# Performance work log

Measured on AMD Instinct MI355X. Metric: run time of the kernel, lower is better.

The kernel has to match this reference:

```python
import jax, jax.numpy as jnp
import numpy as np

DIM = 1024
HEADS = 8
DIM_HEAD = 64
INNER = HEADS * DIM_HEAD
SCALE = DIM_HEAD ** -0.5


def setup_inputs() -> dict:
    key = jax.random.key(0)
    ks = jax.random.split(key, 6)
    b, n = 2, 2048
    x = jax.random.normal(ks[0], (b, n, DIM), dtype=jnp.float32)
    rel_pos_bias = jax.random.normal(ks[1], (HEADS, n, n), dtype=jnp.float32)
    # learned params (Linear stores W as [out, in]; we keep [in, out] for x @ W)
    Wq = jax.random.normal(ks[2], (DIM, INNER), dtype=jnp.float32) * (DIM ** -0.5)
    Wkv = jax.random.normal(ks[3], (DIM, 2 * DIM_HEAD), dtype=jnp.float32) * (DIM ** -0.5)
    Wo = jax.random.normal(ks[4], (INNER, DIM), dtype=jnp.float32) * (INNER ** -0.5)
    bo = jax.random.normal(ks[5], (DIM,), dtype=jnp.float32) * 0.01
    return {"x": x, "rel_pos_bias": rel_pos_bias, "Wq": Wq, "Wkv": Wkv, "Wo": Wo, "bo": bo}


def reference(x, rel_pos_bias, Wq, Wkv, Wo, bo):
    b, n, _ = x.shape
    q = x @ Wq                       # [b, n, h*d]
    kv = x @ Wkv                     # [b, n, 2d] (multi-query: single shared kv head)
    k, v = kv[..., :DIM_HEAD], kv[..., DIM_HEAD:]
    q = q.reshape(b, n, HEADS, DIM_HEAD).transpose(0, 2, 1, 3) * SCALE  # [b, h, n, d]
    sim = jnp.einsum('bhid,bjd->bhij', q, k)
    sim = sim + rel_pos_bias         # bias broadcast over batch
    causal_mask = jnp.triu(jnp.ones((n, n), dtype=bool), k=1)
    neg = -jnp.finfo(sim.dtype).max
    sim = jnp.where(causal_mask, neg, sim)
    attn = jax.nn.softmax(sim, axis=-1)  # stable softmax (max-subtract internally)
    out = jnp.einsum('bhij,bjd->bhid', attn, v)
    out = out.transpose(0, 2, 1, 3).reshape(b, n, INNER)  # [b, n, h*d]
    return out @ Wo + bo
```

## Files before the change

kernel.cpp:

```cpp
#include <hip/hip_runtime.h>

#define NSEQ 2048
#define NB 2
#define NH 8
#define HD 64
#define DMODEL 1024
#define DINNER 512

#define SLOT_F 4224
#define LOG2E 1.44269504f

typedef __attribute__((ext_vector_type(8))) short bf16x8;
typedef __attribute__((ext_vector_type(4))) float f32x4;

__device__ __forceinline__ ushort f2bf(float f) {
  uint u = __float_as_uint(f);
  uint r = (u + 0x7fffu + ((u >> 16) & 1u)) >> 16;
  return (ushort)r;
}

__device__ __forceinline__ void gld16(const ushort* g, ushort* l) {
  __builtin_amdgcn_global_load_lds(
      (const __attribute__((address_space(1))) uint*)g,
      (__attribute__((address_space(3))) uint*)l, 16, 0, 0);
}

__global__ __launch_bounds__(256) void transpose_cast_both_kernel(
    const float* __restrict__ Wq, const float* __restrict__ Wkv,
    const float* __restrict__ Wo, ushort* __restrict__ WT1,
    ushort* __restrict__ WoT) {
  __shared__ float t[64][65];
  const int id = blockIdx.x;
  const float *srcA, *srcB;
  int ldA, ldB, nsplit, Ktot, k0, n0;
  ushort* dst;
  if (id < 160) {
    k0 = (id & 15) * 64; n0 = (id >> 4) * 64;
    srcA = Wq; srcB = Wkv; ldA = 512; ldB = 128; nsplit = 512;
    Ktot = 1024; dst = WT1;
  } else {
    const int u = id - 160;
    k0 = (u & 7) * 64; n0 = (u >> 3) * 64;
    srcA = Wo; srcB = Wo; ldA = 1024; ldB = 1024; nsplit = 1024;
    Ktot = 512; dst = WoT;
  }
  const float* src; int ld, nb;
  if (n0 < nsplit) { src = srcA; ld = ldA; nb = n0; }
  else { src = srcB; ld = ldB; nb = n0 - nsplit; }
  const int r = threadIdx.x >> 4;
  const int c = (threadIdx.x & 15) * 4;
#pragma unroll
  for (int rr = r; rr < 64; rr += 16) {
    float4 v = *(const float4*)(src + (size_t)(k0 + rr) * ld + nb + c);
    t[rr][c + 0] = v.x; t[rr][c + 1] = v.y; t[rr][c + 2] = v.z; t[rr][c + 3] = v.w;
  }
  __syncthreads();
#pragma unroll
  for (int rr = r; rr < 64; rr += 16) {
    ushort4 o;
    o.x = f2bf(t[c + 0][rr]); o.y = f2bf(t[c + 1][rr]);
    o.z = f2bf(t[c + 2][rr]); o.w = f2bf(t[c + 3][rr]);
    *(ushort4*)(dst + (size_t)(n0 + rr) * Ktot + k0 + c) = o;
  }
}

__device__ __forceinline__ void stageA_bf16(const ushort* __restrict__ src, int ld,
                                            int row0, int k0, ushort* lds, int tid) {
#pragma unroll
  for (int i = 0; i < 4; ++i) {
    const int cix = i * 256 + tid;
    const int row = cix >> 3, j = cix & 7;
    uint4 v = *(const uint4*)(src + (size_t)(row0 + row) * ld + k0 + j * 8);
    *(uint4*)((char*)lds + row * 128 + ((j ^ (row & 7)) << 4)) = v;
  }
}
__device__ __forceinline__ void stageA_f32(const float* __restrict__ src, int ld,
                                           int row0, int k0, ushort* lds, int tid) {
#pragma unroll
  for (int i = 0; i < 4; ++i) {
    const int cix = i * 256 + tid;
    const int row = cix >> 3, j = cix & 7;
    const float* p = src + (size_t)(row0 + row) * ld + k0 + j * 8;
    float4 a = *(const float4*)p;
    float4 b = *(const float4*)(p + 4);
    uint u0, u1, u2, u3;
    asm("v_cvt_pk_bf16_f32 %0, %1, %2" : "=v"(u0) : "v"(a.x), "v"(a.y));
    asm("v_cvt_pk_bf16_f32 %0, %1, %2" : "=v"(u1) : "v"(a.z), "v"(a.w));
    asm("v_cvt_pk_bf16_f32 %0, %1, %2" : "=v"(u2) : "v"(b.x), "v"(b.y));
    asm("v_cvt_pk_bf16_f32 %0, %1, %2" : "=v"(u3) : "v"(b.z), "v"(b.w));
    uint4 v; v.x = u0; v.y = u1; v.z = u2; v.w = u3;
    *(uint4*)((char*)lds + row * 128 + ((j ^ (row & 7)) << 4)) = v;
  }
}
__device__ __forceinline__ void stageB(const ushort* __restrict__ src, int ld,
                                       int row0, int k0, ushort* lds, int tid) {
#pragma unroll
  for (int i = 0; i < 2; ++i) {
    const int cix = i * 256 + tid;
    const int row = cix >> 3, j = cix & 7;
    uint4 v = *(const uint4*)(src + (size_t)(row0 + row) * ld + k0 + j * 8);
    *(uint4*)((char*)lds + row * 128 + ((j ^ (row & 7)) << 4)) = v;
  }
}

__global__ __launch_bounds__(256) void qkv_mfma_kernel(
    const float* __restrict__ x, const ushort* __restrict__ WT1,
    ushort* __restrict__ qb, ushort* __restrict__ ksw, ushort* __restrict__ vsw) {
  __shared__ ushort As[128 * 64];
  __shared__ ushort Bs[64 * 64];
  const int tid = threadIdx.x;
  const int m0 = blockIdx.x * 128, n0 = blockIdx.y * 64;
  const int lane = tid & 63;
  const int w = tid >> 6;
  const int wr = w >> 1, wc = w & 1;
  const int lr = lane & 15, lg = lane >> 4;
  f32x4 acc[4][2];
#pragma unroll
  for (int a = 0; a < 4; ++a)
#pragma unroll
    for (int b = 0; b < 2; ++b) acc[a][b] = (f32x4){0.f, 0.f, 0.f, 0.f};
  for (int k0 = 0; k0 < DMODEL; k0 += 64) {
    __syncthreads();
    stageA_f32(x, DMODEL, m0, k0, As, tid);
    stageB(WT1, DMODEL, n0, k0, Bs, tid);
    __syncthreads();
#pragma unroll
    for (int kk = 0; kk < 2; ++kk) {
      bf16x8 af[4], bfr[2];
#pragma unroll
      for (int mi = 0; mi < 4; ++mi) {
        const int r = wr * 64 + mi * 16 + lr;
        af[mi] = *(const bf16x8*)((char*)As + r * 128 + (((kk * 4 + lg) ^ (r & 7)) << 4));
      }
#pragma unroll
      for (int ni = 0; ni < 2; ++ni) {
        const int r = wc * 32 + ni * 16 + lr;
        bfr[ni] = *(const bf16x8*)((char*)Bs + r * 128 + (((kk * 4 + lg) ^ (r & 7)) << 4));
      }
#pragma unroll
      for (int mi = 0; mi < 4; ++mi)
#pragma unroll
        for (int ni = 0; ni < 2; ++ni)
          acc[mi][ni] = __builtin_amdgcn_mfma_f32_16x16x32_bf16(af[mi], bfr[ni],
                                                                acc[mi][ni], 0, 0, 0);
    }
  }
#pragma unroll
  for (int mi = 0; mi < 4; ++mi)
#pragma unroll
    for (int ni = 0; ni < 2; ++ni) {
      const int n = n0 + wc * 32 + ni * 16 + lr;
#pragma unroll
      for (int r = 0; r < 4; ++r) {
        const int m = m0 + wr * 64 + mi * 16 + lg * 4 + r;
        const int bb = m >> 11, key = m & (NSEQ - 1);
        const float v = acc[mi][ni][r];
        if (blockIdx.y < 8) {
          const int h = n >> 6, d = n & 63;
          qb[((size_t)((bb * NH + h) * NSEQ) + key) * HD + d] = f2bf(v * 0.125f);
        } else if (blockIdx.y == 8) {
          const int d = n - DINNER;
          const int t = key >> 6, row = key & 63;
          ksw[(size_t)((bb * 32 + t) * 64 + row) * 64 +
              (((d >> 3) ^ (row & 7)) << 3) + (d & 7)] = f2bf(v);
        } else {
          const int d = n - DINNER - HD;
          const int pr = key >> 7, kk = key & 127;
          vsw[(size_t)((bb * 16 + pr) * 64 + d) * 128 +
              (((kk >> 3) ^ (d & 15)) << 3) + (kk & 7)] = f2bf(v);
        }
      }
    }
}

__global__ __launch_bounds__(256) void out_mfma_kernel(
    const ushort* __restrict__ ab, const ushort* __restrict__ WoT,
    const float* __restrict__ bo, float* __restrict__ out) {
  __shared__ ushort As[128 * 64];
  __shared__ ushort Bs[64 * 64];
  const int tid = threadIdx.x;
  const int m0 = blockIdx.x * 128, n0 = blockIdx.y * 64;
  const int lane = tid & 63;
  const int w = tid >> 6;
  const int wr = w >> 1, wc = w & 1;
  const int lr = lane & 15, lg = lane >> 4;
  f32x4 acc[4][2];
#pragma unroll
  for (int a = 0; a < 4; ++a)
#pragma unroll
    for (int b = 0; b < 2; ++b) acc[a][b] = (f32x4){0.f, 0.f, 0.f, 0.f};
  for (int k0 = 0; k0 < DINNER; k0 += 64) {
    __syncthreads();
    stageA_bf16(ab, DINNER, m0, k0, As, tid);
    stageB(WoT, DINNER, n0, k0, Bs, tid);
    __syncthreads();
#pragma unroll
    for (int kk = 0; kk < 2; ++kk) {
      bf16x8 af[4], bfr[2];
#pragma unroll
      for (int mi = 0; mi < 4; ++mi) {
        const int r = wr * 64 + mi * 16 + lr;
        af[mi] = *(const bf16x8*)((char*)As + r * 128 + (((kk * 4 + lg) ^ (r & 7)) << 4));
      }
#pragma unroll
      for (int ni = 0; ni < 2; ++ni) {
        const int r = wc * 32 + ni * 16 + lr;
        bfr[ni] = *(const bf16x8*)((char*)Bs + r * 128 + (((kk * 4 + lg) ^ (r & 7)) << 4));
      }
#pragma unroll
      for (int mi = 0; mi < 4; ++mi)
#pragma unroll
        for (int ni = 0; ni < 2; ++ni)
          acc[mi][ni] = __builtin_amdgcn_mfma_f32_16x16x32_bf16(af[mi], bfr[ni],
                                                                acc[mi][ni], 0, 0, 0);
    }
  }
#pragma unroll
  for (int mi = 0; mi < 4; ++mi)
#pragma unroll
    for (int ni = 0; ni < 2; ++ni) {
      const int n = n0 + wc * 32 + ni * 16 + lr;
      const float bias = bo[n];
#pragma unroll
      for (int r = 0; r < 4; ++r) {
        const int m = m0 + wr * 64 + mi * 16 + lg * 4 + r;
        out[(size_t)m * DMODEL + n] = acc[mi][ni][r] + bias;
      }
    }
}

__global__ __launch_bounds__(256) void attn_mfma_kernel(
    const ushort* __restrict__ qb, const ushort* __restrict__ ksw,
    const ushort* __restrict__ vsw, const float* __restrict__ rpb,
    ushort* __restrict__ ob, float* __restrict__ scratch) {
  __shared__ ushort Ks[2 * 128 * 64];
  __shared__ ushort Vs[2 * 64 * 128];
  __shared__ ushort Ps[4 * 16 * 128];
  const int tid = threadIdx.x;
  const int lane = tid & 63;
  const int w = tid >> 6;
  const int id = blockIdx.x;
  const int bh = id & 15;
  int qt, ch, p0, p1, partial;
  if (id < 256) {
    qt = 16 + (id >> 4); ch = 0; p0 = 0; p1 = 8; partial = 1;
  } else if (id < 512) {
    qt = 31 - ((id - 256) >> 4); ch = 1; p0 = 8; p1 = (qt >> 1) + 1; partial = 1;
  } else {
    qt = 15 - ((id - 512) >> 4); ch = 0; p0 = 0; p1 = (qt >> 1) + 1; partial = 0;
  }
  const int bb = bh >> 3, h = bh & 7;
  const int q0 = qt * 64;
  const int lr = lane & 15;
  const int lg = lane >> 4;
  const int pdiag = qt >> 1;

  const ushort* kpair = ksw + (size_t)bb * 32 * 64 * 64;
  const ushort* vpair = vsw + (size_t)bb * 16 * 64 * 128;
  const ushort* ksrcw = kpair + w * 2048 + lane * 8;
  const ushort* vsrcw = vpair + w * 2048 + lane * 8;
  ushort* kdstw = Ks + w * 2048;
  ushort* vdstw = Vs + w * 2048;

#define ISSUE(pp, bsel)                                                     \
  {                                                                         \
    const ushort* _ks = ksrcw + (size_t)(pp) * 8192;                        \
    const ushort* _vs = vsrcw + (size_t)(pp) * 8192;                        \
    ushort* _kd = kdstw + (bsel) * 8192;                                    \
    ushort* _vd = vdstw + (bsel) * 8192;                                    \
    gld16(_ks + 0 * 512, _kd + 0 * 512);                                    \
    gld16(_ks + 1 * 512, _kd + 1 * 512);                                    \
    gld16(_ks + 2 * 512, _kd + 2 * 512);                                    \
    gld16(_ks + 3 * 512, _kd + 3 * 512);                                    \
    gld16(_vs + 0 * 512, _vd + 0 * 512);                                    \
    gld16(_vs + 1 * 512, _vd + 1 * 512);                                    \
    gld16(_vs + 2 * 512, _vd + 2 * 512);                                    \
    gld16(_vs + 3 * 512, _vd + 3 * 512);                                    \
  }

#define LOAD_BIAS(pp, dst)                                                  \
  {                                                                         \
    const float* _br = rpb + (size_t)h * NSEQ * NSEQ +                      \
                       (size_t)(q0 + w * 16 + lg * 4) * NSEQ +              \
                       (pp) * 128 + lr;                                     \
    _Pragma("unroll")                                                       \
    for (int _ct = 0; _ct < 8; ++_ct)                                       \
      _Pragma("unroll")                                                     \
      for (int _r = 0; _r < 4; ++_r)                                        \
        dst[_ct][_r] = _br[(size_t)_r * NSEQ + _ct * 16];                   \
  }

  bf16x8 qf[2];
  {
    const ushort* qrow =
        qb + ((size_t)(bh * NSEQ) + q0 + w * 16 + lr) * HD + lg * 8;
    qf[0] = *(const bf16x8*)qrow;
    qf[1] = *(const bf16x8*)(qrow + 32);
  }
  f32x4 oacc[4];
  float m_run[4], l_run[4];
#pragma unroll
  for (int r = 0; r < 4; ++r) { m_run[r] = -1e30f; l_run[r] = 0.f; }
#pragma unroll
  for (int dt = 0; dt < 4; ++dt) oacc[dt] = (f32x4){0.f, 0.f, 0.f, 0.f};

  float bias_c[8][4], bias_n[8][4];

  ISSUE(p0, 0);
  LOAD_BIAS(p0, bias_c);
  ISSUE(p0 + 1, 1);
  int curb = 0;

  for (int p = p0; p < p1; ++p) {
    if (p < p1 - 1) {
      asm volatile("s_waitcnt vmcnt(40)" ::: "memory");
    } else {
      asm volatile("s_waitcnt vmcnt(32)" ::: "memory");
    }
    __builtin_amdgcn_sched_barrier(0);
    __builtin_amdgcn_s_barrier();

    const char* Kc = (const char*)(Ks + curb * 8192);
    const char* Vc = (const char*)(Vs + curb * 8192);
    f32x4 s[8];
    __builtin_amdgcn_s_setprio(1);
#pragma unroll
    for (int ct = 0; ct < 8; ++ct) {
      s[ct] = (f32x4){0.f, 0.f, 0.f, 0.f};
      const int krow = ct * 16 + lr;
#pragma unroll
      for (int kk = 0; kk < 2; ++kk) {
        bf16x8 kf = *(const bf16x8*)(Kc + krow * 128 +
                                     (((kk * 4 + lg) ^ (krow & 7)) << 4));
        s[ct] = __builtin_amdgcn_mfma_f32_16x16x32_bf16(qf[kk], kf, s[ct], 0, 0, 0);
      }
    }
    __builtin_amdgcn_s_setprio(0);
    if (p + 1 < p1) LOAD_BIAS(p + 1, bias_n);
#pragma unroll
    for (int ct = 0; ct < 8; ++ct)
#pragma unroll
      for (int r = 0; r < 4; ++r) s[ct][r] += bias_c[ct][r];
    if (p == pdiag) {
      const int qrel = q0 + w * 16 + lg * 4;
#pragma unroll
      for (int ct = 0; ct < 8; ++ct) {
        const int kg = p * 128 + ct * 16 + lr;
#pragma unroll
        for (int r = 0; r < 4; ++r)
          if (kg > qrel + r) s[ct][r] = -1e30f;
      }
    }
    float fac[4];
#pragma unroll
    for (int r = 0; r < 4; ++r) {
      float mt = s[0][r];
#pragma unroll
      for (int ct = 1; ct < 8; ++ct) mt = fmaxf(mt, s[ct][r]);
#pragma unroll
      for (int msk = 1; msk < 16; msk <<= 1)
        mt = fmaxf(mt, __shfl_xor(mt, msk, 64));
      const float m_new = fmaxf(m_run[r], mt);
      fac[r] = __expf(m_run[r] - m_new);
      m_run[r] = m_new;
      float ls = 0.f;
#pragma unroll
      for (int ct = 0; ct < 8; ++ct) {
        const float pv = __expf(s[ct][r] - m_new);
        s[ct][r] = pv;
        ls += pv;
      }
#pragma unroll
      for (int msk = 1; msk < 16; msk <<= 1) ls += __shfl_xor(ls, msk, 64);
      l_run[r] = l_run[r] * fac[r] + ls;
    }
#pragma unroll
    for (int dt = 0; dt < 4; ++dt)
#pragma unroll
      for (int r = 0; r < 4; ++r) oacc[dt][r] *= fac[r];
    char* Pw = (char*)Ps + w * 4096;
#pragma unroll
    for (int ct = 0; ct < 8; ++ct) {
      uint u01, u23;
      asm("v_cvt_pk_bf16_f32 %0, %1, %2" : "=v"(u01) : "v"(s[ct][0]), "v"(s[ct][1]));
      asm("v_cvt_pk_bf16_f32 %0, %1, %2" : "=v"(u23) : "v"(s[ct][2]), "v"(s[ct][3]));
      const int cbyte = (ct * 16 + lr) * 2;
      const int chv = cbyte >> 4, off = cbyte & 15;
      const int r0 = lg * 4;
      *(ushort*)(Pw + (r0 + 0) * 256 + (((chv ^ (r0 + 0)) << 4) | off)) = (ushort)u01;
      *(ushort*)(Pw + (r0 + 1) * 256 + (((chv ^ (r0 + 1)) << 4) | off)) = (ushort)(u01 >> 16);
      *(ushort*)(Pw + (r0 + 2) * 256 + (((chv ^ (r0 + 2)) << 4) | off)) = (ushort)u23;
      *(ushort*)(Pw + (r0 + 3) * 256 + (((chv ^ (r0 + 3)) << 4) | off)) = (ushort)(u23 >> 16);
    }
    __builtin_amdgcn_s_setprio(1);
#pragma unroll
    for (int kk = 0; kk < 4; ++kk) {
      bf16x8 pf = *(const bf16x8*)(Pw + lr * 256 + (((kk * 4 + lg) ^ lr) << 4));
#pragma unroll
      for (int dt = 0; dt < 4; ++dt) {
        const int vrow = dt * 16 + lr;
        bf16x8 vf = *(const bf16x8*)(Vc + vrow * 256 +
                                     (((kk * 4 + lg) ^ (vrow & 15)) << 4));
        oacc[dt] =
            __builtin_amdgcn_mfma_f32_16x16x32_bf16(pf, vf, oacc[dt], 0, 0, 0);
      }
    }
    __builtin_amdgcn_s_setprio(0);
    __builtin_amdgcn_sched_barrier(0);
    __builtin_amdgcn_s_barrier();
    if (p + 2 < p1) ISSUE(p + 2, curb);
    if (p + 1 < p1) {
#pragma unroll
      for (int ct = 0; ct < 8; ++ct)
#pragma unroll
        for (int r = 0; r < 4; ++r) bias_c[ct][r] = bias_n[ct][r];
    }
    curb ^= 1;
  }
#undef ISSUE
#undef LOAD_BIAS
  if (!partial) {
#pragma unroll
    for (int r = 0; r < 4; ++r) {
      const int qg = q0 + w * 16 + lg * 4 + r;
      const float inv = 1.0f / l_run[r];
      ushort* dst = ob + ((size_t)(bb * NSEQ) + qg) * DINNER + h * HD + lr;
#pragma unroll
      for (int dt = 0; dt < 4; ++dt) dst[dt * 16] = f2bf(oacc[dt][r] * inv);
    }
  } else {
    float* slot =
        scratch + (size_t)((bh * 16 + (qt - 16)) * 2 + ch) * SLOT_F;
#pragma unroll
    for (int r = 0; r < 4; ++r) {
      const int row = w * 16 + lg * 4 + r;
#pragma unroll
      for (int dt = 0; dt < 4; ++dt)
        slot[row * 64 + dt * 16 + lr] = oacc[dt][r];
      if (lr == 0) {
        slot[4096 + row] = m_run[r];
        slot[4160 + row] = l_run[r];
      }
    }
  }
}

__global__ __launch_bounds__(256) void attn_merge_kernel(
    const float* __restrict__ scratch, ushort* __restrict__ ob) {
  const int bid = blockIdx.x;
  const int bh = bid >> 4;
  const int qt = 16 + (bid & 15);
  const int bb = bh >> 3, h = bh & 7;
  const float* s0 = scratch + (size_t)((bh * 16 + (qt - 16)) * 2) * SLOT_F;
  const float* s1 = s0 + SLOT_F;
  const int t = threadIdx.x;
  const int r = t >> 2;
  const int c0 = (t & 3) * 16;
  const float m0 = s0[4096 + r], m1 = s1[4096 + r];
  const float M = fmaxf(m0, m1);
  const float sc0 = __expf(m0 - M), sc1 = __expf(m1 - M);
  const float L = s0[4160 + r] * sc0 + s1[4160 + r] * sc1;
  const float inv = 1.0f / L;
  ushort* dst = ob + ((size_t)(bb * NSEQ) + qt * 64 + r) * DINNER + h * HD + c0;
#pragma unroll
  for (int j4 = 0; j4 < 4; ++j4) {
    float4 a = *(const float4*)(s0 + r * 64 + c0 + j4 * 4);
    float4 b = *(const float4*)(s1 + r * 64 + c0 + j4 * 4);
    dst[j4 * 4 + 0] = f2bf((a.x * sc0 + b.x * sc1) * inv);
    dst[j4 * 4 + 1] = f2bf((a.y * sc0 + b.y * sc1) * inv);
    dst[j4 * 4 + 2] = f2bf((a.z * sc0 + b.z * sc1) * inv);
    dst[j4 * 4 + 3] = f2bf((a.w * sc0 + b.w * sc1) * inv);
  }
}

extern "C" void kernel_launch(void* const* d_in, const int* in_sizes, int n_in,
                              void* d_out, int out_size, void* d_ws, size_t ws_size,
                              hipStream_t stream) {
  (void)in_sizes; (void)n_in; (void)out_size; (void)ws_size;
  const float* x = (const float*)d_in[0];
  const float* rpb = (const float*)d_in[1];
  const float* Wq = (const float*)d_in[2];
  const float* Wkv = (const float*)d_in[3];
  const float* Wo = (const float*)d_in[4];
  const float* bo = (const float*)d_in[5];
  float* out = (float*)d_out;

  ushort* qbb = (ushort*)d_ws;
  ushort* ksw = qbb + (size_t)NB * NH * NSEQ * HD;
  ushort* vsw = ksw + (size_t)NB * NSEQ * HD;
  ushort* obuf = vsw + (size_t)NB * NSEQ * HD;
  ushort* WT1 = obuf + (size_t)NB * NSEQ * DINNER;
  ushort* WoT = WT1 + (size_t)640 * DMODEL;
  float* scratch = (float*)(WoT + (size_t)DMODEL * DINNER);

  transpose_cast_both_kernel<<<dim3(288), 256, 0, stream>>>(Wq, Wkv, Wo, WT1, WoT);
  qkv_mfma_kernel<<<dim3(32, 10), 256, 0, stream>>>(x, WT1, qbb, ksw, vsw);
  attn_mfma_kernel<<<dim3(768), 256, 0, stream>>>(qbb, ksw, vsw, rpb, obuf,
                                                  scratch);
  attn_merge_kernel<<<dim3(256), 256, 0, stream>>>(scratch, obuf);
  out_mfma_kernel<<<dim3(32, 16), 256, 0, stream>>>(obuf, WoT, bo, out);
}
```

Baseline: 82.89 us.

## Pre-swizzle weight and attention-output tiles for direct LDS loads and double-buffer out GEMM

The transpose-cast kernel now writes weights as contiguous 64x64 tiles in the XOR-swizzled order the GEMMs read. The attention and merge kernels likewise write their output as swizzled 128x64 tiles. This lets qkv and out GEMMs stage B (and A in out GEMM) via global_load_lds DMA without going through registers. The out GEMM gains a double-buffered pipeline with vmcnt waits and setprio, at the cost of more LDS and scattered bf16 writes in the attention epilogue.

```diff
diff --git a/kernel.cpp b/kernel.cpp
--- a/kernel.cpp
+++ b/kernel.cpp
@@ -8,7 +8,6 @@
 #define DINNER 512
 
 #define SLOT_F 4224
-#define LOG2E 1.44269504f
 
 typedef __attribute__((ext_vector_type(8))) short bf16x8;
 typedef __attribute__((ext_vector_type(4))) float f32x4;
@@ -27,22 +26,24 @@
 
 __global__ __launch_bounds__(256) void transpose_cast_both_kernel(
     const float* __restrict__ Wq, const float* __restrict__ Wkv,
-    const float* __restrict__ Wo, ushort* __restrict__ WT1,
-    ushort* __restrict__ WoT) {
+    const float* __restrict__ Wo, ushort* __restrict__ WT1sw,
+    ushort* __restrict__ WoTsw) {
   __shared__ float t[64][65];
   const int id = blockIdx.x;
   const float *srcA, *srcB;
-  int ldA, ldB, nsplit, Ktot, k0, n0;
-  ushort* dst;
+  int ldA, ldB, nsplit, k0, n0;
+  ushort* tile;
   if (id < 160) {
-    k0 = (id & 15) * 64; n0 = (id >> 4) * 64;
+    const int nt = id >> 4, kt = id & 15;
+    k0 = kt * 64; n0 = nt * 64;
     srcA = Wq; srcB = Wkv; ldA = 512; ldB = 128; nsplit = 512;
-    Ktot = 1024; dst = WT1;
+    tile = WT1sw + (size_t)(nt * 16 + kt) * 4096;
   } else {
     const int u = id - 160;
-    k0 = (u & 7) * 64; n0 = (u >> 3) * 64;
+    const int nt = u >> 3, kt = u & 7;
+    k0 = kt * 64; n0 = nt * 64;
     srcA = Wo; srcB = Wo; ldA = 1024; ldB = 1024; nsplit = 1024;
-    Ktot = 512; dst = WoT;
+    tile = WoTsw + (size_t)(nt * 8 + kt) * 4096;
   }
   const float* src; int ld, nb;
   if (n0 < nsplit) { src = srcA; ld = ldA; nb = n0; }
@@ -60,20 +61,10 @@
     ushort4 o;
     o.x = f2bf(t[c + 0][rr]); o.y = f2bf(t[c + 1][rr]);
     o.z = f2bf(t[c + 2][rr]); o.w = f2bf(t[c + 3][rr]);
-    *(ushort4*)(dst + (size_t)(n0 + rr) * Ktot + k0 + c) = o;
-  }
-}
-
-__device__ __forceinline__ void stageA_bf16(const ushort* __restrict__ src, int ld,
-                                            int row0, int k0, ushort* lds, int tid) {
-#pragma unroll
-  for (int i = 0; i < 4; ++i) {
-    const int cix = i * 256 + tid;
-    const int row = cix >> 3, j = cix & 7;
-    uint4 v = *(const uint4*)(src + (size_t)(row0 + row) * ld + k0 + j * 8);
-    *(uint4*)((char*)lds + row * 128 + ((j ^ (row & 7)) << 4)) = v;
-  }
-}
+    *(ushort4*)(tile + (size_t)rr * 64 + (((c >> 3) ^ (rr & 7)) << 3) + (c & 7)) = o;
+  }
+}
+
 __device__ __forceinline__ void stageA_f32(const float* __restrict__ src, int ld,
                                            int row0, int k0, ushort* lds, int tid) {
 #pragma unroll
@@ -92,24 +83,15 @@
     *(uint4*)((char*)lds + row * 128 + ((j ^ (row & 7)) << 4)) = v;
   }
 }
-__device__ __forceinline__ void stageB(const ushort* __restrict__ src, int ld,
-                                       int row0, int k0, ushort* lds, int tid) {
-#pragma unroll
-  for (int i = 0; i < 2; ++i) {
-    const int cix = i * 256 + tid;
-    const int row = cix >> 3, j = cix & 7;
-    uint4 v = *(const uint4*)(src + (size_t)(row0 + row) * ld + k0 + j * 8);
-    *(uint4*)((char*)lds + row * 128 + ((j ^ (row & 7)) << 4)) = v;
-  }
-}
 
 __global__ __launch_bounds__(256) void qkv_mfma_kernel(
-    const float* __restrict__ x, const ushort* __restrict__ WT1,
+    const float* __restrict__ x, const ushort* __restrict__ WT1sw,
     ushort* __restrict__ qb, ushort* __restrict__ ksw, ushort* __restrict__ vsw) {
   __shared__ ushort As[128 * 64];
   __shared__ ushort Bs[64 * 64];
   const int tid = threadIdx.x;
-  const int m0 = blockIdx.x * 128, n0 = blockIdx.y * 64;
+  const int m0 = blockIdx.x * 128;
+  const int nt = blockIdx.y;
   const int lane = tid & 63;
   const int w = tid >> 6;
   const int wr = w >> 1, wc = w & 1;
@@ -119,10 +101,15 @@
   for (int a = 0; a < 4; ++a)
 #pragma unroll
     for (int b = 0; b < 2; ++b) acc[a][b] = (f32x4){0.f, 0.f, 0.f, 0.f};
-  for (int k0 = 0; k0 < DMODEL; k0 += 64) {
+  for (int kt = 0; kt < 16; ++kt) {
     __syncthreads();
-    stageA_f32(x, DMODEL, m0, k0, As, tid);
-    stageB(WT1, DMODEL, n0, k0, Bs, tid);
+    {
+      const ushort* bsrc =
+          WT1sw + (size_t)(nt * 16 + kt) * 4096 + w * 1024 + lane * 8;
+      gld16(bsrc, Bs + w * 1024);
+      gld16(bsrc + 512, Bs + w * 1024 + 512);
+    }
+    stageA_f32(x, DMODEL, m0, kt * 64, As, tid);
     __syncthreads();
 #pragma unroll
     for (int kk = 0; kk < 2; ++kk) {
@@ -149,16 +136,16 @@
   for (int mi = 0; mi < 4; ++mi)
 #pragma unroll
     for (int ni = 0; ni < 2; ++ni) {
-      const int n = n0 + wc * 32 + ni * 16 + lr;
+      const int n = nt * 64 + wc * 32 + ni * 16 + lr;
 #pragma unroll
       for (int r = 0; r < 4; ++r) {
         const int m = m0 + wr * 64 + mi * 16 + lg * 4 + r;
         const int bb = m >> 11, key = m & (NSEQ - 1);
         const float v = acc[mi][ni][r];
-        if (blockIdx.y < 8) {
+        if (nt < 8) {
           const int h = n >> 6, d = n & 63;
           qb[((size_t)((bb * NH + h) * NSEQ) + key) * HD + d] = f2bf(v * 0.125f);
-        } else if (blockIdx.y == 8) {
+        } else if (nt == 8) {
           const int d = n - DINNER;
           const int t = key >> 6, row = key & 63;
           ksw[(size_t)((bb * 32 + t) * 64 + row) * 64 +
@@ -174,12 +161,13 @@
 }
 
 __global__ __launch_bounds__(256) void out_mfma_kernel(
-    const ushort* __restrict__ ab, const ushort* __restrict__ WoT,
+    const ushort* __restrict__ obsw, const ushort* __restrict__ WoTsw,
     const float* __restrict__ bo, float* __restrict__ out) {
-  __shared__ ushort As[128 * 64];
-  __shared__ ushort Bs[64 * 64];
+  __shared__ ushort As[2 * 128 * 64];
+  __shared__ ushort Bs[2 * 64 * 64];
   const int tid = threadIdx.x;
-  const int m0 = blockIdx.x * 128, n0 = blockIdx.y * 64;
+  const int mt = blockIdx.x;
+  const int nt = blockIdx.y;
   const int lane = tid & 63;
   const int w = tid >> 6;
   const int wr = w >> 1, wc = w & 1;
@@ -189,23 +177,49 @@
   for (int a = 0; a < 4; ++a)
 #pragma unroll
     for (int b = 0; b < 2; ++b) acc[a][b] = (f32x4){0.f, 0.f, 0.f, 0.f};
-  for (int k0 = 0; k0 < DINNER; k0 += 64) {
-    __syncthreads();
-    stageA_bf16(ab, DINNER, m0, k0, As, tid);
-    stageB(WoT, DINNER, n0, k0, Bs, tid);
-    __syncthreads();
+
+#define OISSUE(kt, buf)                                                       \
+  {                                                                           \
+    const ushort* _as =                                                       \
+        obsw + (size_t)(mt * 8 + (kt)) * 8192 + w * 2048 + lane * 8;          \
+    ushort* _ad = As + (buf) * 8192 + w * 2048;                               \
+    gld16(_as, _ad);                                                          \
+    gld16(_as + 512, _ad + 512);                                              \
+    gld16(_as + 1024, _ad + 1024);                                            \
+    gld16(_as + 1536, _ad + 1536);                                            \
+    const ushort* _bs =                                                       \
+        WoTsw + (size_t)(nt * 8 + (kt)) * 4096 + w * 1024 + lane * 8;         \
+    ushort* _bd = Bs + (buf) * 4096 + w * 1024;                               \
+    gld16(_bs, _bd);                                                          \
+    gld16(_bs + 512, _bd + 512);                                              \
+  }
+
+  OISSUE(0, 0);
+  OISSUE(1, 1);
+  int cur = 0;
+  for (int i = 0; i < 8; ++i) {
+    if (i < 7) {
+      asm volatile("s_waitcnt vmcnt(6)" ::: "memory");
+    } else {
+      asm volatile("s_waitcnt vmcnt(0)" ::: "memory");
+    }
+    __builtin_amdgcn_sched_barrier(0);
+    __builtin_amdgcn_s_barrier();
+    const char* Ac = (const char*)(As + cur * 8192);
+    const char* Bc = (const char*)(Bs + cur * 4096);
+    __builtin_amdgcn_s_setprio(1);
 #pragma unroll
     for (int kk = 0; kk < 2; ++kk) {
       bf16x8 af[4], bfr[2];
 #pragma unroll
       for (int mi = 0; mi < 4; ++mi) {
         const int r = wr * 64 + mi * 16 + lr;
-        af[mi] = *(const bf16x8*)((char*)As + r * 128 + (((kk * 4 + lg) ^ (r & 7)) << 4));
+        af[mi] = *(const bf16x8*)(Ac + r * 128 + (((kk * 4 + lg) ^ (r & 7)) << 4));
       }
 #pragma unroll
       for (int ni = 0; ni < 2; ++ni) {
         const int r = wc * 32 + ni * 16 + lr;
-        bfr[ni] = *(const bf16x8*)((char*)Bs + r * 128 + (((kk * 4 + lg) ^ (r & 7)) << 4));
+        bfr[ni] = *(const bf16x8*)(Bc + r * 128 + (((kk * 4 + lg) ^ (r & 7)) << 4));
       }
 #pragma unroll
       for (int mi = 0; mi < 4; ++mi)
@@ -214,16 +228,22 @@
           acc[mi][ni] = __builtin_amdgcn_mfma_f32_16x16x32_bf16(af[mi], bfr[ni],
                                                                 acc[mi][ni], 0, 0, 0);
     }
-  }
+    __builtin_amdgcn_s_setprio(0);
+    __builtin_amdgcn_sched_barrier(0);
+    __builtin_amdgcn_s_barrier();
+    if (i + 2 < 8) OISSUE(i + 2, cur);
+    cur ^= 1;
+  }
+#undef OISSUE
 #pragma unroll
   for (int mi = 0; mi < 4; ++mi)
 #pragma unroll
     for (int ni = 0; ni < 2; ++ni) {
-      const int n = n0 + wc * 32 + ni * 16 + lr;
+      const int n = nt * 64 + wc * 32 + ni * 16 + lr;
       const float bias = bo[n];
 #pragma unroll
       for (int r = 0; r < 4; ++r) {
-        const int m = m0 + wr * 64 + mi * 16 + lg * 4 + r;
+        const int m = mt * 128 + wr * 64 + mi * 16 + lg * 4 + r;
         out[(size_t)m * DMODEL + n] = acc[mi][ni][r] + bias;
       }
     }
@@ -232,7 +252,7 @@
 __global__ __launch_bounds__(256) void attn_mfma_kernel(
     const ushort* __restrict__ qb, const ushort* __restrict__ ksw,
     const ushort* __restrict__ vsw, const float* __restrict__ rpb,
-    ushort* __restrict__ ob, float* __restrict__ scratch) {
+    ushort* __restrict__ obsw, float* __restrict__ scratch) {
   __shared__ ushort Ks[2 * 128 * 64];
   __shared__ ushort Vs[2 * 64 * 128];
   __shared__ ushort Ps[4 * 16 * 128];
@@ -423,10 +443,16 @@
 #pragma unroll
     for (int r = 0; r < 4; ++r) {
       const int qg = q0 + w * 16 + lg * 4 + r;
+      const int m = bb * NSEQ + qg;
+      const int row = m & 127, mt = m >> 7;
+      const int rs = row & 7;
+      ushort* tb = obsw + (size_t)(mt * 8 + h) * 8192 + row * 64;
       const float inv = 1.0f / l_run[r];
-      ushort* dst = ob + ((size_t)(bb * NSEQ) + qg) * DINNER + h * HD + lr;
-#pragma unroll
-      for (int dt = 0; dt < 4; ++dt) dst[dt * 16] = f2bf(oacc[dt][r] * inv);
+#pragma unroll
+      for (int dt = 0; dt < 4; ++dt) {
+        const int d = dt * 16 + lr;
+        tb[(((d >> 3) ^ rs) << 3) + (d & 7)] = f2bf(oacc[dt][r] * inv);
+      }
     }
   } else {
     float* slot =
@@ -446,7 +472,7 @@
 }
 
 __global__ __launch_bounds__(256) void attn_merge_kernel(
-    const float* __restrict__ scratch, ushort* __restrict__ ob) {
+    const float* __restrict__ scratch, ushort* __restrict__ obsw) {
   const int bid = blockIdx.x;
   const int bh = bid >> 4;
   const int qt = 16 + (bid & 15);
@@ -461,16 +487,22 @@
   const float sc0 = __expf(m0 - M), sc1 = __expf(m1 - M);
   const float L = s0[4160 + r] * sc0 + s1[4160 + r] * sc1;
   const float inv = 1.0f / L;
-  ushort* dst = ob + ((size_t)(bb * NSEQ) + qt * 64 + r) * DINNER + h * HD + c0;
+  ushort tmp[16];
 #pragma unroll
   for (int j4 = 0; j4 < 4; ++j4) {
     float4 a = *(const float4*)(s0 + r * 64 + c0 + j4 * 4);
     float4 b = *(const float4*)(s1 + r * 64 + c0 + j4 * 4);
-    dst[j4 * 4 + 0] = f2bf((a.x * sc0 + b.x * sc1) * inv);
-    dst[j4 * 4 + 1] = f2bf((a.y * sc0 + b.y * sc1) * inv);
-    dst[j4 * 4 + 2] = f2bf((a.z * sc0 + b.z * sc1) * inv);
-    dst[j4 * 4 + 3] = f2bf((a.w * sc0 + b.w * sc1) * inv);
-  }
+    tmp[j4 * 4 + 0] = f2bf((a.x * sc0 + b.x * sc1) * inv);
+    tmp[j4 * 4 + 1] = f2bf((a.y * sc0 + b.y * sc1) * inv);
+    tmp[j4 * 4 + 2] = f2bf((a.z * sc0 + b.z * sc1) * inv);
+    tmp[j4 * 4 + 3] = f2bf((a.w * sc0 + b.w * sc1) * inv);
+  }
+  const int m = bb * NSEQ + qt * 64 + r;
+  const int row = m & 127, mt = m >> 7;
+  const int rs = row & 7;
+  ushort* tb = obsw + (size_t)(mt * 8 + h) * 8192 + row * 64;
+  *(uint4*)(tb + ((((c0 >> 3) + 0) ^ rs) << 3)) = *(const uint4*)&tmp[0];
+  *(uint4*)(tb + ((((c0 >> 3) + 1) ^ rs) << 3)) = *(const uint4*)&tmp[8];
 }
 
 extern "C" void kernel_launch(void* const* d_in, const int* in_sizes, int n_in,
@@ -488,15 +520,16 @@
   ushort* qbb = (ushort*)d_ws;
   ushort* ksw = qbb + (size_t)NB * NH * NSEQ * HD;
   ushort* vsw = ksw + (size_t)NB * NSEQ * HD;
-  ushort* obuf = vsw + (size_t)NB * NSEQ * HD;
-  ushort* WT1 = obuf + (size_t)NB * NSEQ * DINNER;
-  ushort* WoT = WT1 + (size_t)640 * DMODEL;
-  float* scratch = (float*)(WoT + (size_t)DMODEL * DINNER);
-
-  transpose_cast_both_kernel<<<dim3(288), 256, 0, stream>>>(Wq, Wkv, Wo, WT1, WoT);
-  qkv_mfma_kernel<<<dim3(32, 10), 256, 0, stream>>>(x, WT1, qbb, ksw, vsw);
-  attn_mfma_kernel<<<dim3(768), 256, 0, stream>>>(qbb, ksw, vsw, rpb, obuf,
+  ushort* obsw = vsw + (size_t)NB * NSEQ * HD;
+  ushort* WT1sw = obsw + (size_t)NB * NSEQ * DINNER;
+  ushort* WoTsw = WT1sw + (size_t)640 * DMODEL;
+  float* scratch = (float*)(WoTsw + (size_t)DMODEL * DINNER);
+
+  transpose_cast_both_kernel<<<dim3(288), 256, 0, stream>>>(Wq, Wkv, Wo, WT1sw,
+                                                            WoTsw);
+  qkv_mfma_kernel<<<dim3(32, 10), 256, 0, stream>>>(x, WT1sw, qbb, ksw, vsw);
+  attn_mfma_kernel<<<dim3(768), 256, 0, stream>>>(qbb, ksw, vsw, rpb, obsw,
                                                   scratch);
-  attn_merge_kernel<<<dim3(256), 256, 0, stream>>>(scratch, obuf);
-  out_mfma_kernel<<<dim3(32, 16), 256, 0, stream>>>(obuf, WoT, bo, out);
-}
+  attn_merge_kernel<<<dim3(256), 256, 0, stream>>>(scratch, obsw);
+  out_mfma_kernel<<<dim3(32, 16), 256, 0, stream>>>(obsw, WoTsw, bo, out);
+}
```

Result: no change. 83.04 us (+0.2%).
